# Kernel tuning notes

Measured on AMD Instinct MI355X. Metric: run time of the kernel, lower is better.

The kernel has to match this reference:

```python
import jax, jax.numpy as jnp
import numpy as np

N_NODES = 100000
N_EDGES = 400000
IN_DIM = 771
HID = 256
N_GRAPHS = 64
EPS = 1e-5


def setup_inputs() -> dict:
    key = jax.random.key(0)
    ks = jax.random.split(key, 24)
    x = jax.random.normal(ks[0], (N_NODES, IN_DIM), dtype=jnp.float32)
    edge_index = jax.random.randint(ks[1], (2, N_EDGES), 0, N_NODES, dtype=jnp.int64)
    batch = jnp.sort(jax.random.randint(ks[2], (N_NODES,), 0, N_GRAPHS, dtype=jnp.int64))
    inp = {"x": x, "edge_index": edge_index, "batch": batch}
    dims = [IN_DIM, HID, HID]
    ki = 3
    for i, din in enumerate(dims):
        s = 1.0 / np.sqrt(din)
        inp[f"Wl{i}"] = jax.random.normal(ks[ki], (din, HID), dtype=jnp.float32) * s; ki += 1
        inp[f"bl{i}"] = jnp.zeros((HID,), dtype=jnp.float32)
        inp[f"Wr{i}"] = jax.random.normal(ks[ki], (din, HID), dtype=jnp.float32) * s; ki += 1
        inp[f"g{i}"] = jnp.ones((HID,), dtype=jnp.float32)
        inp[f"b{i}"] = jnp.zeros((HID,), dtype=jnp.float32)
    # attention pooling: Linear(HID, HID//2) -> Tanh -> Linear(HID//2, 1)
    inp["Wa1"] = jax.random.normal(ks[ki], (HID, HID // 2), dtype=jnp.float32) * (1.0 / np.sqrt(HID)); ki += 1
    inp["ba1"] = jnp.zeros((HID // 2,), dtype=jnp.float32)
    inp["Wa2"] = jax.random.normal(ks[ki], (HID // 2, 1), dtype=jnp.float32) * (1.0 / np.sqrt(HID // 2)); ki += 1
    inp["ba2"] = jnp.zeros((1,), dtype=jnp.float32)
    # classifier: Linear(HID, HID//2) -> ReLU -> Linear(HID//2, 1)
    inp["Wc1"] = jax.random.normal(ks[ki], (HID, HID // 2), dtype=jnp.float32) * (1.0 / np.sqrt(HID)); ki += 1
    inp["bc1"] = jnp.zeros((HID // 2,), dtype=jnp.float32)
    inp["Wc2"] = jax.random.normal(ks[ki], (HID // 2, 1), dtype=jnp.float32) * (1.0 / np.sqrt(HID // 2)); ki += 1
    inp["bc2"] = jnp.zeros((1,), dtype=jnp.float32)
    return inp


def _sage_layer(h, src, dst, Wl, bl, Wr, g, b):
    # SAGEConv(aggr='mean'): out = lin_l(mean_{j->i} x_j) + lin_r(x_i)
    msum = jax.ops.segment_sum(h[src], dst, num_segments=N_NODES)  # [N, d]
    deg = jax.ops.segment_sum(jnp.ones((src.shape[0],), h.dtype), dst, num_segments=N_NODES)
    agg = msum / jnp.maximum(deg, 1.0)[:, None]
    out = agg @ Wl + bl + h @ Wr
    # BatchNorm1d (training-mode batch stats), eval dropout (identity)
    mean = out.mean(axis=0)
    var = out.var(axis=0)
    out = (out - mean) * jax.lax.rsqrt(var + EPS) * g + b
    return jax.nn.relu(out)


def reference(x, edge_index, batch,
              Wl0, bl0, Wr0, g0, b0,
              Wl1, bl1, Wr1, g1, b1,
              Wl2, bl2, Wr2, g2, b2,
              Wa1, ba1, Wa2, ba2,
              Wc1, bc1, Wc2, bc2):
    src, dst = edge_index[0], edge_index[1]
    h = _sage_layer(x, src, dst, Wl0, bl0, Wr0, g0, b0)
    h = _sage_layer(h, src, dst, Wl1, bl1, Wr1, g1, b1)
    h = _sage_layer(h, src, dst, Wl2, bl2, Wr2, g2, b2)
    # attention pooling: per-graph softmax over node scores, weighted sum
    s = (jnp.tanh(h @ Wa1 + ba1) @ Wa2 + ba2)[:, 0]  # [N]
    smax = jax.ops.segment_max(s, batch, num_segments=N_GRAPHS)
    e = jnp.exp(s - smax[batch])
    denom = jax.ops.segment_sum(e, batch, num_segments=N_GRAPHS)
    w = e / denom[batch]
    pooled = jax.ops.segment_sum(h * w[:, None], batch, num_segments=N_GRAPHS)  # [G, HID]
    out = jax.nn.relu(pooled @ Wc1 + bc1) @ Wc2 + bc2  # [G, 1]
    return out[:, 0]
```

## Files before the change

kernel.cpp:

```cpp
#include <hip/hip_runtime.h>
#include <math.h>
#include <stdint.h>

#define HID 256
#define NGRAPH 64
typedef unsigned short ushort_t;

typedef __attribute__((ext_vector_type(8))) short short8;
typedef __attribute__((ext_vector_type(4))) float f32x4;

__device__ __forceinline__ void split2(float v, ushort_t& h, ushort_t& l) {
  unsigned u = __float_as_uint(v);
  unsigned hr = u + 0x7FFFu + ((u >> 16) & 1u);
  h = (ushort_t)(hr >> 16);
  float hf = __uint_as_float(((unsigned)h) << 16);
  float r = v - hf;
  unsigned u2 = __float_as_uint(r);
  unsigned lr = u2 + 0x7FFFu + ((u2 >> 16) & 1u);
  l = (ushort_t)(lr >> 16);
}

#define GLDS(g, l) \
  __builtin_amdgcn_global_load_lds((const __attribute__((address_space(1))) void*)(g), \
                                   (__attribute__((address_space(3))) void*)(l), 16, 0, 0)

__global__ __launch_bounds__(256) void mfma_gemm_kernel(
    const ushort_t* __restrict__ Ah, const ushort_t* __restrict__ Al,
    const ushort_t* __restrict__ Bh, const ushort_t* __restrict__ Bl,
    float* __restrict__ C, int Mrows, int N, int Kpad) {
  __shared__ ushort_t lAh[128 * 32];
  __shared__ ushort_t lAl[128 * 32];
  __shared__ ushort_t lBh[128 * 32];
  __shared__ ushort_t lBl[128 * 32];
  const int tid = threadIdx.x;
  const int m0 = blockIdx.y * 128;
  const int n0 = blockIdx.x * 128;
  const int w = tid >> 6, lane = tid & 63;
  const int wm = (w >> 1) * 64, wn = (w & 1) * 64;
  const int col = lane & 15, quad = lane >> 4;

  f32x4 acc[4][4];
#pragma unroll
  for (int i = 0; i < 4; ++i)
#pragma unroll
    for (int j = 0; j < 4; ++j) acc[i][j] = (f32x4)(0.f);

  for (int kt = 0; kt < Kpad; kt += 32) {
#pragma unroll
    for (int j = 0; j < 2; ++j) {
      const int ch = tid + j * 256;
      const int r = ch >> 2, c = ch & 3;
      const size_t goA = (size_t)(m0 + r) * Kpad + kt + c * 8;
      const size_t goB = (size_t)(n0 + r) * Kpad + kt + c * 8;
      GLDS(Ah + goA, &lAh[ch * 8]);
      GLDS(Al + goA, &lAl[ch * 8]);
      GLDS(Bh + goB, &lBh[ch * 8]);
      GLDS(Bl + goB, &lBl[ch * 8]);
    }
    __syncthreads();
    short8 ah[4], al[4], bh[4], bl[4];
#pragma unroll
    for (int i = 0; i < 4; ++i) {
      const int ar = wm + i * 16 + col;
      ah[i] = *(const short8*)&lAh[ar * 32 + quad * 8];
      al[i] = *(const short8*)&lAl[ar * 32 + quad * 8];
      const int br = wn + i * 16 + col;
      bh[i] = *(const short8*)&lBh[br * 32 + quad * 8];
      bl[i] = *(const short8*)&lBl[br * 32 + quad * 8];
    }
    __syncthreads();
#pragma unroll
    for (int i = 0; i < 4; ++i)
#pragma unroll
      for (int j = 0; j < 4; ++j) {
        acc[i][j] = __builtin_amdgcn_mfma_f32_16x16x32_bf16(ah[i], bh[j], acc[i][j], 0, 0, 0);
        acc[i][j] = __builtin_amdgcn_mfma_f32_16x16x32_bf16(ah[i], bl[j], acc[i][j], 0, 0, 0);
        acc[i][j] = __builtin_amdgcn_mfma_f32_16x16x32_bf16(al[i], bh[j], acc[i][j], 0, 0, 0);
      }
  }
#pragma unroll
  for (int i = 0; i < 4; ++i) {
    const int r0 = m0 + wm + i * 16 + quad * 4;
#pragma unroll
    for (int j = 0; j < 4; ++j) {
      const int cc = n0 + wn + j * 16 + col;
#pragma unroll
      for (int r = 0; r < 4; ++r)
        if (r0 + r < Mrows) C[(size_t)(r0 + r) * N + cc] = acc[i][j][r];
    }
  }
}

__global__ __launch_bounds__(256) void convert_x_kernel(
    const float* __restrict__ x, int row0, int nrows,
    ushort_t* __restrict__ xh, ushort_t* __restrict__ xl, int K, int Kpad) {
  const int perRow = Kpad / 4;
  const int t = blockIdx.x * blockDim.x + threadIdx.x;
  if (t >= nrows * perRow) return;
  const int r = t / perRow, k0 = (t % perRow) * 4;
  const float* xr = x + (size_t)(row0 + r) * K;
  ushort_t h[4], l[4];
#pragma unroll
  for (int i = 0; i < 4; ++i) {
    const float v = (k0 + i < K) ? xr[k0 + i] : 0.f;
    split2(v, h[i], l[i]);
  }
  const size_t o = (size_t)r * Kpad + k0;
  *(ushort4*)(xh + o) = make_ushort4(h[0], h[1], h[2], h[3]);
  *(ushort4*)(xl + o) = make_ushort4(l[0], l[1], l[2], l[3]);
}

__global__ void convert_wt_kernel(const float* __restrict__ W, ushort_t* __restrict__ wth,
                                  ushort_t* __restrict__ wtl, int K, int N, int Kpad) {
  const int t = blockIdx.x * blockDim.x + threadIdx.x;
  if (t >= N * Kpad) return;
  const int n = t / Kpad, k = t % Kpad;
  const float v = (k < K) ? W[(size_t)k * N + n] : 0.f;
  ushort_t h, l;
  split2(v, h, l);
  wth[t] = h;
  wtl[t] = l;
}

__global__ void deg_count_kernel(const int* __restrict__ dst, int* __restrict__ degi, int nE) {
  int e = blockIdx.x * blockDim.x + threadIdx.x;
  if (e < nE) atomicAdd(&degi[dst[e]], 1);
}

__global__ __launch_bounds__(1024) void scan_kernel(const int* __restrict__ degi,
                                                    int* __restrict__ rowptr, int M) {
  __shared__ int part[1024];
  const int t = threadIdx.x;
  const int chunk = (M + 1023) / 1024;
  const int b0 = min(t * chunk, M);
  const int b1 = min(b0 + chunk, M);
  int s = 0;
  for (int i = b0; i < b1; ++i) s += degi[i];
  part[t] = s;
  __syncthreads();
  for (int off = 1; off < 1024; off <<= 1) {
    int v = (t >= off) ? part[t - off] : 0;
    __syncthreads();
    part[t] += v;
    __syncthreads();
  }
  int ex = (t == 0) ? 0 : part[t - 1];
  for (int i = b0; i < b1; ++i) {
    rowptr[i] = ex;
    ex += degi[i];
  }
  if (t == 1023) rowptr[M] = part[1023];
}

__global__ void fill_kernel(const int* __restrict__ src, const int* __restrict__ dst,
                            int* __restrict__ fill, const int* __restrict__ rowptr,
                            int* __restrict__ csr_src, int nE) {
  int e = blockIdx.x * blockDim.x + threadIdx.x;
  if (e >= nE) return;
  const int d = dst[e];
  const int pos = rowptr[d] + atomicAdd(&fill[d], 1);
  csr_src[pos] = src[e];
}

#define GNB 64
__global__ __launch_bounds__(256) void gather_combine_kernel(
    const float* __restrict__ hl, const float* hr,
    const int* __restrict__ rowptr, const int* __restrict__ csr_src,
    const float* __restrict__ bl, float* preBN,
    float* __restrict__ bsum, float* __restrict__ bsumsq, int M) {
  __shared__ float lsum[4][HID];
  __shared__ float lsq[4][HID];
  const int w = threadIdx.x >> 6;
  const int lane = threadIdx.x & 63;
  const float4 blv = ((const float4*)bl)[lane];
  float4 s = make_float4(0.f, 0.f, 0.f, 0.f);
  float4 q = make_float4(0.f, 0.f, 0.f, 0.f);
  const int base = blockIdx.x * GNB;
  for (int it = 0; it < GNB / 4; ++it) {
    const int n = base + it * 4 + w;
    if (n < M) {
      const int e0 = rowptr[n], e1 = rowptr[n + 1];
      float4 acc = make_float4(0.f, 0.f, 0.f, 0.f);
      for (int e = e0; e < e1; ++e) {
        const int sn = csr_src[e];
        const float4 v = ((const float4*)(hl + (size_t)sn * HID))[lane];
        acc.x += v.x; acc.y += v.y; acc.z += v.z; acc.w += v.w;
      }
      const float rd = 1.0f / fmaxf((float)(e1 - e0), 1.0f);
      const float4 hv = ((const float4*)(hr + (size_t)n * HID))[lane];
      float4 o;
      o.x = fmaf(acc.x, rd, blv.x + hv.x);
      o.y = fmaf(acc.y, rd, blv.y + hv.y);
      o.z = fmaf(acc.z, rd, blv.z + hv.z);
      o.w = fmaf(acc.w, rd, blv.w + hv.w);
      ((float4*)(preBN + (size_t)n * HID))[lane] = o;
      s.x += o.x; s.y += o.y; s.z += o.z; s.w += o.w;
      q.x = fmaf(o.x, o.x, q.x); q.y = fmaf(o.y, o.y, q.y);
      q.z = fmaf(o.z, o.z, q.z); q.w = fmaf(o.w, o.w, q.w);
    }
  }
  *(float4*)&lsum[w][lane * 4] = s;
  *(float4*)&lsq[w][lane * 4] = q;
  __syncthreads();
  const int c = threadIdx.x;
  const float ts = lsum[0][c] + lsum[1][c] + lsum[2][c] + lsum[3][c];
  const float tq = lsq[0][c] + lsq[1][c] + lsq[2][c] + lsq[3][c];
  atomicAdd(&bsum[c], ts);
  atomicAdd(&bsumsq[c], tq);
}

__global__ void bn_finalize_kernel(const float* __restrict__ bsum, const float* __restrict__ bsumsq,
                                   const float* __restrict__ g, const float* __restrict__ b,
                                   float* __restrict__ scale, float* __restrict__ shift, int M) {
  const int c = threadIdx.x;
  const float inv = 1.0f / (float)M;
  const float mean = bsum[c] * inv;
  const float var = bsumsq[c] * inv - mean * mean;
  const float rstd = rsqrtf(var + 1e-5f);
  const float sc = g[c] * rstd;
  scale[c] = sc;
  shift[c] = b[c] - mean * sc;
}

__global__ __launch_bounds__(256) void bn_apply_relu_convert_kernel(
    const float* __restrict__ preBN, const float* __restrict__ scale, const float* __restrict__ shift,
    ushort_t* __restrict__ hh, ushort_t* __restrict__ hl, float* __restrict__ hout, int n4) {
  const int i = blockIdx.x * blockDim.x + threadIdx.x;
  if (i >= n4) return;
  const int c4 = i & (HID / 4 - 1);
  const float4 v = ((const float4*)preBN)[i];
  const float4 sc = ((const float4*)scale)[c4];
  const float4 sh = ((const float4*)shift)[c4];
  float o[4];
  o[0] = fmaxf(fmaf(v.x, sc.x, sh.x), 0.f);
  o[1] = fmaxf(fmaf(v.y, sc.y, sh.y), 0.f);
  o[2] = fmaxf(fmaf(v.z, sc.z, sh.z), 0.f);
  o[3] = fmaxf(fmaf(v.w, sc.w, sh.w), 0.f);
  ushort_t h[4], l[4];
#pragma unroll
  for (int k = 0; k < 4; ++k) split2(o[k], h[k], l[k]);
  ((ushort4*)hh)[i] = make_ushort4(h[0], h[1], h[2], h[3]);
  ((ushort4*)hl)[i] = make_ushort4(l[0], l[1], l[2], l[3]);
  if (hout) ((float4*)hout)[i] = make_float4(o[0], o[1], o[2], o[3]);
}

__global__ __launch_bounds__(256) void att_score_kernel(
    const float* __restrict__ t, const float* __restrict__ ba1, const float* __restrict__ Wa2,
    const float* __restrict__ ba2, float* __restrict__ s, int M) {
  const int wid = (blockIdx.x * blockDim.x + threadIdx.x) >> 6;
  const int lane = threadIdx.x & 63;
  if (wid >= M) return;
  const float* row = t + (size_t)wid * 128;
  float acc = tanhf(row[lane] + ba1[lane]) * Wa2[lane] +
              tanhf(row[lane + 64] + ba1[lane + 64]) * Wa2[lane + 64];
#pragma unroll
  for (int off = 32; off > 0; off >>= 1) acc += __shfl_down(acc, off, 64);
  if (lane == 0) s[wid] = acc + ba2[0];
}

__device__ __forceinline__ unsigned fflip(float f) {
  unsigned u = __float_as_uint(f);
  return (u & 0x80000000u) ? ~u : (u | 0x80000000u);
}
__device__ __forceinline__ float funflip(unsigned u) {
  return __uint_as_float((u & 0x80000000u) ? (u ^ 0x80000000u) : ~u);
}

__global__ void seg_max_kernel(const float* __restrict__ s, const int* __restrict__ batch,
                               unsigned* __restrict__ gmax, int M) {
  __shared__ unsigned lmax[NGRAPH];
  if (threadIdx.x < NGRAPH) lmax[threadIdx.x] = 0u;
  __syncthreads();
  for (int i = blockIdx.x * blockDim.x + threadIdx.x; i < M; i += gridDim.x * blockDim.x)
    atomicMax(&lmax[batch[i]], fflip(s[i]));
  __syncthreads();
  if (threadIdx.x < NGRAPH && lmax[threadIdx.x] != 0u) atomicMax(&gmax[threadIdx.x], lmax[threadIdx.x]);
}

__global__ void seg_expsum_kernel(const float* __restrict__ s, const int* __restrict__ batch,
                                  const unsigned* __restrict__ gmax, float* __restrict__ e,
                                  float* __restrict__ denom, int M) {
  __shared__ float ld[NGRAPH];
  if (threadIdx.x < NGRAPH) ld[threadIdx.x] = 0.f;
  __syncthreads();
  for (int i = blockIdx.x * blockDim.x + threadIdx.x; i < M; i += gridDim.x * blockDim.x) {
    const int b = batch[i];
    const float v = expf(s[i] - funflip(gmax[b]));
    e[i] = v;
    atomicAdd(&ld[b], v);
  }
  __syncthreads();
  if (threadIdx.x < NGRAPH && ld[threadIdx.x] != 0.f) atomicAdd(&denom[threadIdx.x], ld[threadIdx.x]);
}

#define PNB 16
__global__ __launch_bounds__(256) void pool_kernel(
    const float* __restrict__ h, const float* __restrict__ e, const float* __restrict__ denom,
    const int* __restrict__ batch, float* __restrict__ pooled, int M) {
  const int wid = (blockIdx.x * blockDim.x + threadIdx.x) >> 6;
  const int lane = threadIdx.x & 63;
  const int n0 = wid * PNB;
  if (n0 >= M) return;
  const int n1 = min(n0 + PNB, M);
  float4 acc = make_float4(0.f, 0.f, 0.f, 0.f);
  int cur = batch[n0];
  for (int n = n0; n < n1; ++n) {
    const int b = batch[n];
    if (b != cur) {
      float* o = pooled + (size_t)cur * HID + lane * 4;
      atomicAdd(o + 0, acc.x); atomicAdd(o + 1, acc.y);
      atomicAdd(o + 2, acc.z); atomicAdd(o + 3, acc.w);
      acc = make_float4(0.f, 0.f, 0.f, 0.f);
      cur = b;
    }
    const float w = e[n] / denom[b];
    const float4 v = ((const float4*)(h + (size_t)n * HID))[lane];
    acc.x = fmaf(v.x, w, acc.x); acc.y = fmaf(v.y, w, acc.y);
    acc.z = fmaf(v.z, w, acc.z); acc.w = fmaf(v.w, w, acc.w);
  }
  float* o = pooled + (size_t)cur * HID + lane * 4;
  atomicAdd(o + 0, acc.x); atomicAdd(o + 1, acc.y);
  atomicAdd(o + 2, acc.z); atomicAdd(o + 3, acc.w);
}

__global__ __launch_bounds__(128) void classifier_kernel(
    const float* __restrict__ pooled, const float* __restrict__ Wc1, const float* __restrict__ bc1,
    const float* __restrict__ Wc2, const float* __restrict__ bc2, float* __restrict__ out) {
  __shared__ float red[128];
  const int g = blockIdx.x;
  const int j = threadIdx.x;
  float acc = bc1[j];
  const float* p = pooled + (size_t)g * HID;
  for (int c = 0; c < HID; ++c) acc = fmaf(p[c], Wc1[c * 128 + j], acc);
  red[j] = fmaxf(acc, 0.f) * Wc2[j];
  __syncthreads();
  for (int off = 64; off > 0; off >>= 1) {
    if (j < off) red[j] += red[j + off];
    __syncthreads();
  }
  if (j == 0) out[g] = red[0] + bc2[0];
}

extern "C" void kernel_launch(void* const* d_in, const int* in_sizes, int n_in,
                              void* d_out, int out_size, void* d_ws, size_t ws_size,
                              hipStream_t stream) {
  const float* x = (const float*)d_in[0];
  const int* edge = (const int*)d_in[1];
  const int* batch = (const int*)d_in[2];
  const int M = in_sizes[2];
  const int nE = in_sizes[1] / 2;
  const int IN_DIM = in_sizes[0] / M;
  const int* src = edge;
  const int* dst = edge + nE;

  const size_t MN = (size_t)M * HID;
  const int Mpad = ((M + 127) / 128) * 128;
  const int KP0 = ((IN_DIM + 31) / 32) * 32;
  const int Mc = 25088;

  float* ws = (float*)d_ws;
  float* buf0 = ws;
  float* buf1 = buf0 + MN;
  float* buf2 = buf1 + MN;
  float* bsum = buf2 + MN;
  float* bsumsq = bsum + HID;
  float* scale = bsumsq + HID;
  float* shift = scale + HID;
  float* ssc = shift + HID;
  float* ew = ssc + M;
  unsigned* gmax = (unsigned*)(ew + M);
  float* denom = (float*)(gmax + NGRAPH);
  float* pooled = denom + NGRAPH;
  int* degi = (int*)(pooled + (size_t)NGRAPH * HID);
  int* filla = degi + M;
  int* rowptr = filla + M;
  int* csr_src = rowptr + M + 1;

  ushort_t* wp = (ushort_t*)(((uintptr_t)(csr_src + nE) + 15) & ~(uintptr_t)15);
  const size_t W0SZ = (size_t)HID * KP0;
  const size_t W1SZ = (size_t)HID * HID;
  const size_t WASZ = (size_t)128 * HID;
  ushort_t* wlh[3], *wll[3], *wrh[3], *wrl[3];
  ushort_t* p = wp;
  for (int l = 0; l < 3; ++l) {
    const size_t sz = (l == 0) ? W0SZ : W1SZ;
    wlh[l] = p; p += sz;
    wll[l] = p; p += sz;
    wrh[l] = p; p += sz;
    wrl[l] = p; p += sz;
  }
  ushort_t* wah = p; p += WASZ;
  ushort_t* wal = p; p += WASZ;
  ushort_t* cvh = (ushort_t*)(((uintptr_t)p + 15) & ~(uintptr_t)15);
  size_t CONVHALF = (size_t)Mc * KP0;
  if ((size_t)Mpad * HID > CONVHALF) CONVHALF = (size_t)Mpad * HID;
  ushort_t* cvl = cvh + CONVHALF;

  hipMemsetAsync(degi, 0, (size_t)(2 * M) * sizeof(int), stream);
  deg_count_kernel<<<(nE + 255) / 256, 256, 0, stream>>>(dst, degi, nE);
  scan_kernel<<<1, 1024, 0, stream>>>(degi, rowptr, M);
  fill_kernel<<<(nE + 255) / 256, 256, 0, stream>>>(src, dst, filla, rowptr, csr_src, nE);
  hipMemsetAsync(gmax, 0, (size_t)(NGRAPH * 2 + NGRAPH * HID) * 4, stream);

  for (int l = 0; l < 3; ++l) {
    const int K = (l == 0) ? IN_DIM : HID;
    const int KP = (l == 0) ? KP0 : HID;
    const float* Wl = (const float*)d_in[3 + l * 5 + 0];
    const float* Wr = (const float*)d_in[3 + l * 5 + 2];
    const int nt = HID * KP;
    convert_wt_kernel<<<(nt + 255) / 256, 256, 0, stream>>>(Wl, wlh[l], wll[l], K, HID, KP);
    convert_wt_kernel<<<(nt + 255) / 256, 256, 0, stream>>>(Wr, wrh[l], wrl[l], K, HID, KP);
  }
  convert_wt_kernel<<<(128 * HID + 255) / 256, 256, 0, stream>>>(
      (const float*)d_in[18], wah, wal, HID, 128, HID);

  const int n4 = (int)(MN / 4);
  for (int l = 0; l < 3; ++l) {
    const float* bl = (const float*)d_in[3 + l * 5 + 1];
    const float* gg = (const float*)d_in[3 + l * 5 + 3];
    const float* bb = (const float*)d_in[3 + l * 5 + 4];
    float* gl = (l == 0) ? buf0 : (l == 1) ? buf1 : buf2;
    float* gr = (l == 0) ? buf1 : (l == 1) ? buf2 : buf0;
    float* pb = (l == 0) ? buf2 : (l == 1) ? buf0 : buf1;

    if (l == 0) {
      for (int c0 = 0; c0 < M; c0 += Mc) {
        const int rows = min(Mc, M - c0);
        const int nt = rows * (KP0 / 4);
        convert_x_kernel<<<(nt + 255) / 256, 256, 0, stream>>>(x, c0, rows, cvh, cvl, IN_DIM, KP0);
        dim3 g(HID / 128, (rows + 127) / 128);
        mfma_gemm_kernel<<<g, 256, 0, stream>>>(cvh, cvl, wlh[0], wll[0],
                                                gl + (size_t)c0 * HID, rows, HID, KP0);
        mfma_gemm_kernel<<<g, 256, 0, stream>>>(cvh, cvl, wrh[0], wrl[0],
                                                gr + (size_t)c0 * HID, rows, HID, KP0);
      }
    } else {
      dim3 g(HID / 128, (M + 127) / 128);
      mfma_gemm_kernel<<<g, 256, 0, stream>>>(cvh, cvl, wlh[l], wll[l], gl, M, HID, HID);
      mfma_gemm_kernel<<<g, 256, 0, stream>>>(cvh, cvl, wrh[l], wrl[l], gr, M, HID, HID);
    }
    hipMemsetAsync(bsum, 0, HID * 2 * sizeof(float), stream);
    gather_combine_kernel<<<(M + GNB - 1) / GNB, 256, 0, stream>>>(
        gl, gr, rowptr, csr_src, bl, pb, bsum, bsumsq, M);
    bn_finalize_kernel<<<1, HID, 0, stream>>>(bsum, bsumsq, gg, bb, scale, shift, M);
    bn_apply_relu_convert_kernel<<<(n4 + 255) / 256, 256, 0, stream>>>(
        pb, scale, shift, cvh, cvl, (l == 2) ? gl : nullptr, n4);
  }
  const float* h = buf2;
  float* tbuf = buf0;

  {
    dim3 g(1, (M + 127) / 128);
    mfma_gemm_kernel<<<g, 256, 0, stream>>>(cvh, cvl, wah, wal, tbuf, M, 128, HID);
  }
  att_score_kernel<<<(M * 64 + 255) / 256, 256, 0, stream>>>(
      tbuf, (const float*)d_in[19], (const float*)d_in[20], (const float*)d_in[21], ssc, M);
  seg_max_kernel<<<512, 256, 0, stream>>>(ssc, batch, gmax, M);
  seg_expsum_kernel<<<512, 256, 0, stream>>>(ssc, batch, gmax, ew, denom, M);
  {
    const int nwaves = (M + PNB - 1) / PNB;
    pool_kernel<<<(nwaves * 64 + 255) / 256, 256, 0, stream>>>(h, ew, denom, batch, pooled, M);
  }
  classifier_kernel<<<NGRAPH, 128, 0, stream>>>(
      pooled, (const float*)d_in[22], (const float*)d_in[23],
      (const float*)d_in[24], (const float*)d_in[25], (float*)d_out);
}
```

Measured before the change: 2.143 ms.

## Concatenate Wl/Wr into one GEMM, fuse attention epilogue and BN finalize

Packs Wl and Wr side by side into a single 512-wide weight matrix, so each layer runs one GEMM that writes an interleaved buffer and reads A once instead of twice. Converts x in a single full pass rather than in chunks. Fuses the tanh/dot attention scoring into the attention GEMM epilogue and folds BN finalize into the apply kernel. This removes kernel launches and A-matrix re-reads, at the cost of a larger workspace and a strided 512-wide layout that the gather must now read.

Result: faster. 2.100 ms (-2.0%).

```diff
diff --git a/kernel.cpp b/kernel.cpp
--- a/kernel.cpp
+++ b/kernel.cpp
@@ -24,10 +24,10 @@
   __builtin_amdgcn_global_load_lds((const __attribute__((address_space(1))) void*)(g), \
                                    (__attribute__((address_space(3))) void*)(l), 16, 0, 0)
 
-__global__ __launch_bounds__(256) void mfma_gemm_kernel(
+__global__ __launch_bounds__(256) void mfma_gemm512_kernel(
     const ushort_t* __restrict__ Ah, const ushort_t* __restrict__ Al,
     const ushort_t* __restrict__ Bh, const ushort_t* __restrict__ Bl,
-    float* __restrict__ C, int Mrows, int N, int Kpad) {
+    float* __restrict__ C, int Mrows, int Kpad) {
   __shared__ ushort_t lAh[128 * 32];
   __shared__ ushort_t lAl[128 * 32];
   __shared__ ushort_t lBh[128 * 32];
@@ -86,19 +86,109 @@
       const int cc = n0 + wn + j * 16 + col;
 #pragma unroll
       for (int r = 0; r < 4; ++r)
-        if (r0 + r < Mrows) C[(size_t)(r0 + r) * N + cc] = acc[i][j][r];
-    }
+        if (r0 + r < Mrows) C[(size_t)(r0 + r) * 512 + cc] = acc[i][j][r];
+    }
+  }
+}
+
+__global__ __launch_bounds__(256) void mfma_att_kernel(
+    const ushort_t* __restrict__ Ah, const ushort_t* __restrict__ Al,
+    const ushort_t* __restrict__ Bh, const ushort_t* __restrict__ Bl,
+    const float* __restrict__ ba1, const float* __restrict__ Wa2,
+    const float* __restrict__ ba2, float* __restrict__ S, int Mrows, int Kpad) {
+  __shared__ ushort_t lAh[128 * 32];
+  __shared__ ushort_t lAl[128 * 32];
+  __shared__ ushort_t lBh[128 * 32];
+  __shared__ ushort_t lBl[128 * 32];
+  __shared__ float sat[128][2];
+  const int tid = threadIdx.x;
+  const int m0 = blockIdx.y * 128;
+  const int w = tid >> 6, lane = tid & 63;
+  const int wm = (w >> 1) * 64, wn = (w & 1) * 64;
+  const int col = lane & 15, quad = lane >> 4;
+
+  f32x4 acc[4][4];
+#pragma unroll
+  for (int i = 0; i < 4; ++i)
+#pragma unroll
+    for (int j = 0; j < 4; ++j) acc[i][j] = (f32x4)(0.f);
+
+  for (int kt = 0; kt < Kpad; kt += 32) {
+#pragma unroll
+    for (int j = 0; j < 2; ++j) {
+      const int ch = tid + j * 256;
+      const int r = ch >> 2, c = ch & 3;
+      const size_t goA = (size_t)(m0 + r) * Kpad + kt + c * 8;
+      const size_t goB = (size_t)r * Kpad + kt + c * 8;
+      GLDS(Ah + goA, &lAh[ch * 8]);
+      GLDS(Al + goA, &lAl[ch * 8]);
+      GLDS(Bh + goB, &lBh[ch * 8]);
+      GLDS(Bl + goB, &lBl[ch * 8]);
+    }
+    __syncthreads();
+    short8 ah[4], al[4], bh[4], bl[4];
+#pragma unroll
+    for (int i = 0; i < 4; ++i) {
+      const int ar = wm + i * 16 + col;
+      ah[i] = *(const short8*)&lAh[ar * 32 + quad * 8];
+      al[i] = *(const short8*)&lAl[ar * 32 + quad * 8];
+      const int br = wn + i * 16 + col;
+      bh[i] = *(const short8*)&lBh[br * 32 + quad * 8];
+      bl[i] = *(const short8*)&lBl[br * 32 + quad * 8];
+    }
+    __syncthreads();
+#pragma unroll
+    for (int i = 0; i < 4; ++i)
+#pragma unroll
+      for (int j = 0; j < 4; ++j) {
+        acc[i][j] = __builtin_amdgcn_mfma_f32_16x16x32_bf16(ah[i], bh[j], acc[i][j], 0, 0, 0);
+        acc[i][j] = __builtin_amdgcn_mfma_f32_16x16x32_bf16(ah[i], bl[j], acc[i][j], 0, 0, 0);
+        acc[i][j] = __builtin_amdgcn_mfma_f32_16x16x32_bf16(al[i], bh[j], acc[i][j], 0, 0, 0);
+      }
+  }
+  float part[4][4];
+#pragma unroll
+  for (int i = 0; i < 4; ++i)
+#pragma unroll
+    for (int r = 0; r < 4; ++r) part[i][r] = 0.f;
+#pragma unroll
+  for (int j = 0; j < 4; ++j) {
+    const int cc = wn + j * 16 + col;
+    const float a1 = ba1[cc];
+    const float w2 = Wa2[cc];
+#pragma unroll
+    for (int i = 0; i < 4; ++i)
+#pragma unroll
+      for (int r = 0; r < 4; ++r)
+        part[i][r] += tanhf(acc[i][j][r] + a1) * w2;
+  }
+#pragma unroll
+  for (int mask = 1; mask < 16; mask <<= 1)
+#pragma unroll
+    for (int i = 0; i < 4; ++i)
+#pragma unroll
+      for (int r = 0; r < 4; ++r) part[i][r] += __shfl_xor(part[i][r], mask, 64);
+  if (col == 0) {
+#pragma unroll
+    for (int i = 0; i < 4; ++i)
+#pragma unroll
+      for (int r = 0; r < 4; ++r) sat[wm + i * 16 + quad * 4 + r][wn >> 6] = part[i][r];
+  }
+  __syncthreads();
+  if (tid < 128) {
+    const int gm = m0 + tid;
+    if (gm < Mrows) S[gm] = sat[tid][0] + sat[tid][1] + ba2[0];
   }
 }
 
 __global__ __launch_bounds__(256) void convert_x_kernel(
-    const float* __restrict__ x, int row0, int nrows,
+    const float* __restrict__ x, int nrows,
     ushort_t* __restrict__ xh, ushort_t* __restrict__ xl, int K, int Kpad) {
   const int perRow = Kpad / 4;
   const int t = blockIdx.x * blockDim.x + threadIdx.x;
   if (t >= nrows * perRow) return;
   const int r = t / perRow, k0 = (t % perRow) * 4;
-  const float* xr = x + (size_t)(row0 + r) * K;
+  const float* xr = x + (size_t)r * K;
   ushort_t h[4], l[4];
 #pragma unroll
   for (int i = 0; i < 4; ++i) {
@@ -110,12 +200,14 @@
   *(ushort4*)(xl + o) = make_ushort4(l[0], l[1], l[2], l[3]);
 }
 
-__global__ void convert_wt_kernel(const float* __restrict__ W, ushort_t* __restrict__ wth,
-                                  ushort_t* __restrict__ wtl, int K, int N, int Kpad) {
+__global__ void convert_wt_kernel(const float* __restrict__ W1, const float* __restrict__ W2,
+                                  ushort_t* __restrict__ wth, ushort_t* __restrict__ wtl,
+                                  int K, int Kpad, int ntot, int ld) {
   const int t = blockIdx.x * blockDim.x + threadIdx.x;
-  if (t >= N * Kpad) return;
+  if (t >= ntot * Kpad) return;
   const int n = t / Kpad, k = t % Kpad;
-  const float v = (k < K) ? W[(size_t)k * N + n] : 0.f;
+  float v = 0.f;
+  if (k < K) v = (n < 256) ? W1[(size_t)k * ld + n] : W2[(size_t)k * ld + (n - 256)];
   ushort_t h, l;
   split2(v, h, l);
   wth[t] = h;
@@ -164,7 +256,7 @@
 
 #define GNB 64
 __global__ __launch_bounds__(256) void gather_combine_kernel(
-    const float* __restrict__ hl, const float* hr,
+    const float* __restrict__ gbuf,
     const int* __restrict__ rowptr, const int* __restrict__ csr_src,
     const float* __restrict__ bl, float* preBN,
     float* __restrict__ bsum, float* __restrict__ bsumsq, int M) {
@@ -183,11 +275,11 @@
       float4 acc = make_float4(0.f, 0.f, 0.f, 0.f);
       for (int e = e0; e < e1; ++e) {
         const int sn = csr_src[e];
-        const float4 v = ((const float4*)(hl + (size_t)sn * HID))[lane];
+        const float4 v = ((const float4*)(gbuf + (size_t)sn * 512))[lane];
         acc.x += v.x; acc.y += v.y; acc.z += v.z; acc.w += v.w;
       }
       const float rd = 1.0f / fmaxf((float)(e1 - e0), 1.0f);
-      const float4 hv = ((const float4*)(hr + (size_t)n * HID))[lane];
+      const float4 hv = ((const float4*)(gbuf + (size_t)n * 512 + 256))[lane];
       float4 o;
       o.x = fmaf(acc.x, rd, blv.x + hv.x);
       o.y = fmaf(acc.y, rd, blv.y + hv.y);
@@ -209,53 +301,37 @@
   atomicAdd(&bsumsq[c], tq);
 }
 
-__global__ void bn_finalize_kernel(const float* __restrict__ bsum, const float* __restrict__ bsumsq,
-                                   const float* __restrict__ g, const float* __restrict__ b,
-                                   float* __restrict__ scale, float* __restrict__ shift, int M) {
-  const int c = threadIdx.x;
-  const float inv = 1.0f / (float)M;
-  const float mean = bsum[c] * inv;
-  const float var = bsumsq[c] * inv - mean * mean;
-  const float rstd = rsqrtf(var + 1e-5f);
-  const float sc = g[c] * rstd;
-  scale[c] = sc;
-  shift[c] = b[c] - mean * sc;
-}
-
 __global__ __launch_bounds__(256) void bn_apply_relu_convert_kernel(
-    const float* __restrict__ preBN, const float* __restrict__ scale, const float* __restrict__ shift,
-    ushort_t* __restrict__ hh, ushort_t* __restrict__ hl, float* __restrict__ hout, int n4) {
+    const float* __restrict__ preBN, const float* __restrict__ bsum,
+    const float* __restrict__ bsumsq, const float* __restrict__ g, const float* __restrict__ b,
+    ushort_t* __restrict__ hh, ushort_t* __restrict__ hl, float* __restrict__ hout,
+    int M, int n4) {
+  __shared__ float s_sc[HID], s_sh[HID];
+  {
+    const int c = threadIdx.x;
+    const float inv = 1.0f / (float)M;
+    const float mean = bsum[c] * inv;
+    const float var = bsumsq[c] * inv - mean * mean;
+    const float sc = g[c] * rsqrtf(var + 1e-5f);
+    s_sc[c] = sc;
+    s_sh[c] = b[c] - mean * sc;
+  }
+  __syncthreads();
   const int i = blockIdx.x * blockDim.x + threadIdx.x;
   if (i >= n4) return;
-  const int c4 = i & (HID / 4 - 1);
+  const int c0 = (i & (HID / 4 - 1)) * 4;
   const float4 v = ((const float4*)preBN)[i];
-  const float4 sc = ((const float4*)scale)[c4];
-  const float4 sh = ((const float4*)shift)[c4];
   float o[4];
-  o[0] = fmaxf(fmaf(v.x, sc.x, sh.x), 0.f);
-  o[1] = fmaxf(fmaf(v.y, sc.y, sh.y), 0.f);
-  o[2] = fmaxf(fmaf(v.z, sc.z, sh.z), 0.f);
-  o[3] = fmaxf(fmaf(v.w, sc.w, sh.w), 0.f);
+  o[0] = fmaxf(fmaf(v.x, s_sc[c0 + 0], s_sh[c0 + 0]), 0.f);
+  o[1] = fmaxf(fmaf(v.y, s_sc[c0 + 1], s_sh[c0 + 1]), 0.f);
+  o[2] = fmaxf(fmaf(v.z, s_sc[c0 + 2], s_sh[c0 + 2]), 0.f);
+  o[3] = fmaxf(fmaf(v.w, s_sc[c0 + 3], s_sh[c0 + 3]), 0.f);
   ushort_t h[4], l[4];
 #pragma unroll
   for (int k = 0; k < 4; ++k) split2(o[k], h[k], l[k]);
   ((ushort4*)hh)[i] = make_ushort4(h[0], h[1], h[2], h[3]);
   ((ushort4*)hl)[i] = make_ushort4(l[0], l[1], l[2], l[3]);
   if (hout) ((float4*)hout)[i] = make_float4(o[0], o[1], o[2], o[3]);
-}
-
-__global__ __launch_bounds__(256) void att_score_kernel(
-    const float* __restrict__ t, const float* __restrict__ ba1, const float* __restrict__ Wa2,
-    const float* __restrict__ ba2, float* __restrict__ s, int M) {
-  const int wid = (blockIdx.x * blockDim.x + threadIdx.x) >> 6;
-  const int lane = threadIdx.x & 63;
-  if (wid >= M) return;
-  const float* row = t + (size_t)wid * 128;
-  float acc = tanhf(row[lane] + ba1[lane]) * Wa2[lane] +
-              tanhf(row[lane + 64] + ba1[lane + 64]) * Wa2[lane + 64];
-#pragma unroll
-  for (int off = 32; off > 0; off >>= 1) acc += __shfl_down(acc, off, 64);
-  if (lane == 0) s[wid] = acc + ba2[0];
 }
 
 __device__ __forceinline__ unsigned fflip(float f) {
@@ -353,22 +429,18 @@
   const int* src = edge;
   const int* dst = edge + nE;
 
-  const size_t MN = (size_t)M * HID;
   const int Mpad = ((M + 127) / 128) * 128;
   const int KP0 = ((IN_DIM + 31) / 32) * 32;
-  const int Mc = 25088;
+  const int mblocks = (M + 127) / 128;
 
   float* ws = (float*)d_ws;
-  float* buf0 = ws;
-  float* buf1 = buf0 + MN;
-  float* buf2 = buf1 + MN;
-  float* bsum = buf2 + MN;
-  float* bsumsq = bsum + HID;
-  float* scale = bsumsq + HID;
-  float* shift = scale + HID;
-  float* ssc = shift + HID;
+  float* gbuf = ws;
+  float* pbuf = gbuf + (size_t)M * 512;
+  float* h32 = pbuf + (size_t)M * HID;
+  float* ssc = h32 + (size_t)M * HID;
   float* ew = ssc + M;
-  unsigned* gmax = (unsigned*)(ew + M);
+  float* bsumA = ew + M;
+  unsigned* gmax = (unsigned*)(bsumA + 6 * HID);
   float* denom = (float*)(gmax + NGRAPH);
   float* pooled = denom + NGRAPH;
   int* degi = (int*)(pooled + (size_t)NGRAPH * HID);
@@ -377,89 +449,67 @@
   int* csr_src = rowptr + M + 1;
 
   ushort_t* wp = (ushort_t*)(((uintptr_t)(csr_src + nE) + 15) & ~(uintptr_t)15);
-  const size_t W0SZ = (size_t)HID * KP0;
-  const size_t W1SZ = (size_t)HID * HID;
-  const size_t WASZ = (size_t)128 * HID;
-  ushort_t* wlh[3], *wll[3], *wrh[3], *wrl[3];
-  ushort_t* p = wp;
-  for (int l = 0; l < 3; ++l) {
-    const size_t sz = (l == 0) ? W0SZ : W1SZ;
-    wlh[l] = p; p += sz;
-    wll[l] = p; p += sz;
-    wrh[l] = p; p += sz;
-    wrl[l] = p; p += sz;
-  }
-  ushort_t* wah = p; p += WASZ;
-  ushort_t* wal = p; p += WASZ;
-  ushort_t* cvh = (ushort_t*)(((uintptr_t)p + 15) & ~(uintptr_t)15);
-  size_t CONVHALF = (size_t)Mc * KP0;
-  if ((size_t)Mpad * HID > CONVHALF) CONVHALF = (size_t)Mpad * HID;
-  ushort_t* cvl = cvh + CONVHALF;
+  ushort_t* w0h = wp;                 ushort_t* w0l = w0h + (size_t)512 * KP0;
+  ushort_t* w1h = w0l + (size_t)512 * KP0;  ushort_t* w1l = w1h + (size_t)512 * HID;
+  ushort_t* w2h = w1l + (size_t)512 * HID;  ushort_t* w2l = w2h + (size_t)512 * HID;
+  ushort_t* wah = w2l + (size_t)512 * HID;  ushort_t* wal = wah + (size_t)128 * HID;
+  ushort_t* cvh = (ushort_t*)(((uintptr_t)(wal + (size_t)128 * HID) + 15) & ~(uintptr_t)15);
+  ushort_t* cvl = cvh + (size_t)Mpad * KP0;
 
   hipMemsetAsync(degi, 0, (size_t)(2 * M) * sizeof(int), stream);
   deg_count_kernel<<<(nE + 255) / 256, 256, 0, stream>>>(dst, degi, nE);
   scan_kernel<<<1, 1024, 0, stream>>>(degi, rowptr, M);
   fill_kernel<<<(nE + 255) / 256, 256, 0, stream>>>(src, dst, filla, rowptr, csr_src, nE);
-  hipMemsetAsync(gmax, 0, (size_t)(NGRAPH * 2 + NGRAPH * HID) * 4, stream);
-
+  hipMemsetAsync(bsumA, 0, (size_t)(6 * HID + 2 * NGRAPH + NGRAPH * HID) * 4, stream);
+
+  {
+    const int nt0 = 512 * KP0;
+    convert_wt_kernel<<<(nt0 + 255) / 256, 256, 0, stream>>>(
+        (const float*)d_in[3], (const float*)d_in[5], w0h, w0l, IN_DIM, KP0, 512, HID);
+    const int nt1 = 512 * HID;
+    convert_wt_kernel<<<(nt1 + 255) / 256, 256, 0, stream>>>(
+        (const float*)d_in[8], (const float*)d_in[10], w1h, w1l, HID, HID, 512, HID);
+    convert_wt_kernel<<<(nt1 + 255) / 256, 256, 0, stream>>>(
+        (const float*)d_in[13], (const float*)d_in[15], w2h, w2l, HID, HID, 512, HID);
+    convert_wt_kernel<<<(128 * HID + 255) / 256, 256, 0, stream>>>(
+        (const float*)d_in[18], nullptr, wah, wal, HID, HID, 128, 128);
+  }
+
+  {
+    const int nt = M * (KP0 / 4);
+    convert_x_kernel<<<(nt + 255) / 256, 256, 0, stream>>>(x, M, cvh, cvl, IN_DIM, KP0);
+  }
+
+  const int n4 = (int)((size_t)M * HID / 4);
+  const ushort_t* WH[3] = {w0h, w1h, w2h};
+  const ushort_t* WL[3] = {w0l, w1l, w2l};
   for (int l = 0; l < 3; ++l) {
-    const int K = (l == 0) ? IN_DIM : HID;
     const int KP = (l == 0) ? KP0 : HID;
-    const float* Wl = (const float*)d_in[3 + l * 5 + 0];
-    const float* Wr = (const float*)d_in[3 + l * 5 + 2];
-    const int nt = HID * KP;
-    convert_wt_kernel<<<(nt + 255) / 256, 256, 0, stream>>>(Wl, wlh[l], wll[l], K, HID, KP);
-    convert_wt_kernel<<<(nt + 255) / 256, 256, 0, stream>>>(Wr, wrh[l], wrl[l], K, HID, KP);
-  }
-  convert_wt_kernel<<<(128 * HID + 255) / 256, 256, 0, stream>>>(
-      (const float*)d_in[18], wah, wal, HID, 128, HID);
-
-  const int n4 = (int)(MN / 4);
-  for (int l = 0; l < 3; ++l) {
     const float* bl = (const float*)d_in[3 + l * 5 + 1];
     const float* gg = (const float*)d_in[3 + l * 5 + 3];
     const float* bb = (const float*)d_in[3 + l * 5 + 4];
-    float* gl = (l == 0) ? buf0 : (l == 1) ? buf1 : buf2;
-    float* gr = (l == 0) ? buf1 : (l == 1) ? buf2 : buf0;
-    float* pb = (l == 0) ? buf2 : (l == 1) ? buf0 : buf1;
-
-    if (l == 0) {
-      for (int c0 = 0; c0 < M; c0 += Mc) {
-        const int rows = min(Mc, M - c0);
-        const int nt = rows * (KP0 / 4);
-        convert_x_kernel<<<(nt + 255) / 256, 256, 0, stream>>>(x, c0, rows, cvh, cvl, IN_DIM, KP0);
-        dim3 g(HID / 128, (rows + 127) / 128);
-        mfma_gemm_kernel<<<g, 256, 0, stream>>>(cvh, cvl, wlh[0], wll[0],
-                                                gl + (size_t)c0 * HID, rows, HID, KP0);
-        mfma_gemm_kernel<<<g, 256, 0, stream>>>(cvh, cvl, wrh[0], wrl[0],
-                                                gr + (size_t)c0 * HID, rows, HID, KP0);
-      }
-    } else {
-      dim3 g(HID / 128, (M + 127) / 128);
-      mfma_gemm_kernel<<<g, 256, 0, stream>>>(cvh, cvl, wlh[l], wll[l], gl, M, HID, HID);
-      mfma_gemm_kernel<<<g, 256, 0, stream>>>(cvh, cvl, wrh[l], wrl[l], gr, M, HID, HID);
-    }
-    hipMemsetAsync(bsum, 0, HID * 2 * sizeof(float), stream);
+    float* bsum = bsumA + l * 512;
+    float* bsumsq = bsum + HID;
+
+    dim3 g(4, mblocks);
+    mfma_gemm512_kernel<<<g, 256, 0, stream>>>(cvh, cvl, WH[l], WL[l], gbuf, M, KP);
     gather_combine_kernel<<<(M + GNB - 1) / GNB, 256, 0, stream>>>(
-        gl, gr, rowptr, csr_src, bl, pb, bsum, bsumsq, M);
-    bn_finalize_kernel<<<1, HID, 0, stream>>>(bsum, bsumsq, gg, bb, scale, shift, M);
+        gbuf, rowptr, csr_src, bl, pbuf, bsum, bsumsq, M);
     bn_apply_relu_convert_kernel<<<(n4 + 255) / 256, 256, 0, stream>>>(
-        pb, scale, shift, cvh, cvl, (l == 2) ? gl : nullptr, n4);
-  }
-  const float* h = buf2;
-  float* tbuf = buf0;
+        pbuf, bsum, bsumsq, gg, bb, cvh, cvl, (l == 2) ? h32 : nullptr, M, n4);
+  }
 
   {
-    dim3 g(1, (M + 127) / 128);
-    mfma_gemm_kernel<<<g, 256, 0, stream>>>(cvh, cvl, wah, wal, tbuf, M, 128, HID);
-  }
-  att_score_kernel<<<(M * 64 + 255) / 256, 256, 0, stream>>>(
-      tbuf, (const float*)d_in[19], (const float*)d_in[20], (const float*)d_in[21], ssc, M);
+    dim3 g(1, mblocks);
+    mfma_att_kernel<<<g, 256, 0, stream>>>(
+        cvh, cvl, wah, wal, (const float*)d_in[19], (const float*)d_in[20],
+        (const float*)d_in[21], ssc, M, HID);
+  }
   seg_max_kernel<<<512, 256, 0, stream>>>(ssc, batch, gmax, M);
   seg_expsum_kernel<<<512, 256, 0, stream>>>(ssc, batch, gmax, ew, denom, M);
   {
     const int nwaves = (M + PNB - 1) / PNB;
-    pool_kernel<<<(nwaves * 64 + 255) / 256, 256, 0, stream>>>(h, ew, denom, batch, pooled, M);
+    pool_kernel<<<(nwaves * 64 + 255) / 256, 256, 0, stream>>>(h32, ew, denom, batch, pooled, M);
   }
   classifier_kernel<<<NGRAPH, 128, 0, stream>>>(
       pooled, (const float*)d_in[22], (const float*)d_in[23],
```
